# Kernel optimization log

Measured on AMD Instinct MI355X. Metric: run time of the kernel, lower is better.

## Reference

```python
import jax, jax.numpy as jnp
import numpy as np


def setup_inputs() -> dict:
    key = jax.random.key(0)
    ks = jax.random.split(key, 5)
    B, N, F, S = 8, 128, 32, 8
    F_ = 32          # output channels
    H = 32           # kernel_network hidden width
    node_features = jax.random.normal(ks[0], (B, N, F), dtype=jnp.float32)
    fltr = jax.random.uniform(ks[1], (B, N, N), dtype=jnp.float32)
    edge_features = jax.random.normal(ks[2], (B, N, N, S), dtype=jnp.float32)
    W0 = jax.random.normal(ks[3], (S, H), dtype=jnp.float32) * (1.0 / np.sqrt(S))
    b0 = jnp.zeros((H,), dtype=jnp.float32)
    W_out = jax.random.normal(ks[4], (H, F_ * F), dtype=jnp.float32) * (1.0 / np.sqrt(H))
    b_out = jnp.zeros((F_ * F,), dtype=jnp.float32)
    bias = jnp.zeros((F_,), dtype=jnp.float32)
    return {"node_features": node_features, "fltr": fltr, "edge_features": edge_features,
            "W0": W0, "b0": b0, "W_out": W_out, "b_out": b_out, "bias": bias}


def reference(node_features, fltr, edge_features, W0, b0, W_out, b_out, bias):
    B, N, F = node_features.shape
    F_ = bias.shape[0]
    # row-normalize the filter (adjacency)
    fltr_n = fltr / jnp.maximum(jnp.sum(fltr, axis=-1, keepdims=True), 1e-11)
    # kernel-generating network over edge features: (B,N,N,S) -> (B,N,N,F_*F)
    h = jax.nn.relu(edge_features @ W0 + b0)
    kernel = (h @ W_out + b_out).reshape(B, N, N, F_, F)
    # scale by normalized filter and aggregate neighbors:
    # out[a,b,c] = sum_{i,f} fltr_n[a,b,i] * kernel[a,b,i,c,f] * nf[a,i,f]
    out = jnp.einsum('abi,abicf,aif->abc', fltr_n, kernel, node_features)
    out = out + bias  # (B,N,F_)
    return out
```

## Files before the change

kernel.cpp:

```cpp
#include <hip/hip_runtime.h>

#define Bn 8
#define Nn 128
#define Fdim 32
#define Sdim 8
#define Hdim 32
#define Fout 32

typedef float  f32x4  __attribute__((ext_vector_type(4)));
typedef short  bf16x8 __attribute__((ext_vector_type(8)));

#define PITCH 136

__device__ __forceinline__ unsigned short f2bf(float x) {
    union { float f; unsigned u; } v; v.f = x;
    return (unsigned short)((v.u + 0x7FFFu + ((v.u >> 16) & 1u)) >> 16);
}
__device__ __forceinline__ unsigned pack2(float lo, float hi) {
    return (unsigned)f2bf(lo) | ((unsigned)f2bf(hi) << 16);
}

__global__ __launch_bounds__(256, 4) void ecc_kernel(
    const float* __restrict__ nf,
    const float* __restrict__ fltr,
    const float* __restrict__ ef,
    const float* __restrict__ W0,
    const float* __restrict__ b0,
    const float* __restrict__ Wout,
    const float* __restrict__ bout,
    const float* __restrict__ bias,
    float* __restrict__ out)
{
    __shared__ __align__(16) unsigned short hT[Hdim * PITCH];
    __shared__ __align__(16) unsigned short nT[Fdim * PITCH];
    __shared__ __align__(16) float Ts[Hdim * 36];
    __shared__ __align__(16) float qp[Nn];
    __shared__ float inv_s;

    const int t    = threadIdx.x;
    const int blk  = blockIdx.x;
    const int a    = blk >> 7;
    const int hcol = t & 31;

    const float* __restrict__ nfa  = nf   + (size_t)a   * (Nn * Fdim);
    const float* __restrict__ frow = fltr + (size_t)blk * Nn;
    const float* __restrict__ erow = ef   + (size_t)blk * (Nn * Sdim);

    float w0r[Sdim];
    #pragma unroll
    for (int s = 0; s < Sdim; ++s) w0r[s] = W0[s * Hdim + hcol];
    const float b0r = b0[hcol];

    if (t < 64) {
        float s = frow[t] + frow[t + 64];
        #pragma unroll
        for (int off = 32; off > 0; off >>= 1) s += __shfl_down(s, off);
        if (t == 0) inv_s = 1.0f / fmaxf(s, 1e-11f);
    }

    {
        const int f = t & 31, iseg = t >> 5;
        unsigned* dst = (unsigned*)&nT[f * PITCH + iseg * 16];
        #pragma unroll 4
        for (int k = 0; k < 16; k += 2) {
            const int i = iseg * 16 + k;
            const float x0 = nfa[i * Fdim + f];
            const float x1 = nfa[(i + 1) * Fdim + f];
            dst[k >> 1] = pack2(x0, x1);
        }
    }

    {
        const int il = t >> 5;
        unsigned* dst = (unsigned*)&hT[hcol * PITCH + il * 16];
        #pragma unroll 2
        for (int k = 0; k < 16; k += 2) {
            const int i0 = il * 16 + k;
            const float4 e0a = *(const float4*)(erow + i0 * Sdim);
            const float4 e0b = *(const float4*)(erow + i0 * Sdim + 4);
            const float4 e1a = *(const float4*)(erow + i0 * Sdim + 8);
            const float4 e1b = *(const float4*)(erow + i0 * Sdim + 12);
            float a0 = b0r, a1 = b0r;
            a0 += e0a.x * w0r[0] + e0a.y * w0r[1] + e0a.z * w0r[2] + e0a.w * w0r[3];
            a0 += e0b.x * w0r[4] + e0b.y * w0r[5] + e0b.z * w0r[6] + e0b.w * w0r[7];
            a1 += e1a.x * w0r[0] + e1a.y * w0r[1] + e1a.z * w0r[2] + e1a.w * w0r[3];
            a1 += e1b.x * w0r[4] + e1b.y * w0r[5] + e1b.z * w0r[6] + e1b.w * w0r[7];
            const float h0 = fmaxf(a0, 0.0f) * frow[i0];
            const float h1 = fmaxf(a1, 0.0f) * frow[i0 + 1];
            dst[k >> 1] = pack2(h0, h1);
        }
    }

    if (t >= 128) {
        const int f = t & 31, qr = (t >> 5) & 3;
        float q = 0.f;
        #pragma unroll 4
        for (int k = 0; k < 32; ++k) {
            const int i = qr * 32 + k;
            q += frow[i] * nfa[i * Fdim + f];
        }
        qp[qr * 32 + f] = q;
    }
    __syncthreads();

    {
        const int w  = t >> 6, l = t & 63;
        const int lr = l & 15, lg = l >> 4;
        const int mt = w >> 1, nt = w & 1;
        f32x4 acc = {0.f, 0.f, 0.f, 0.f};
        #pragma unroll
        for (int kt = 0; kt < 4; ++kt) {
            const bf16x8 av = *(const bf16x8*)&hT[(mt * 16 + lr) * PITCH + kt * 32 + lg * 8];
            const bf16x8 bv = *(const bf16x8*)&nT[(nt * 16 + lr) * PITCH + kt * 32 + lg * 8];
            acc = __builtin_amdgcn_mfma_f32_16x16x32_bf16(av, bv, acc, 0, 0, 0);
        }
        #pragma unroll
        for (int r = 0; r < 4; ++r)
            Ts[(mt * 16 + lg * 4 + r) * 36 + nt * 16 + lr] = acc[r];
    }
    __syncthreads();

    {
        const int c = t >> 3, f4 = t & 7;
        const float* wbase = Wout + (size_t)c * Fdim + f4 * 4;
        float partial = 0.f;
        #pragma unroll 8
        for (int h = 0; h < Hdim; ++h) {
            const float4 wv = *(const float4*)(wbase + (size_t)h * (Fout * Fdim));
            const float4 tv = *(const float4*)&Ts[h * 36 + f4 * 4];
            partial += tv.x * wv.x + tv.y * wv.y + tv.z * wv.z + tv.w * wv.w;
        }
        {
            const float4 q0 = *(const float4*)&qp[f4 * 4];
            const float4 q1 = *(const float4*)&qp[32 + f4 * 4];
            const float4 q2 = *(const float4*)&qp[64 + f4 * 4];
            const float4 q3 = *(const float4*)&qp[96 + f4 * 4];
            const float4 bv = *(const float4*)(bout + (size_t)c * Fdim + f4 * 4);
            partial += (q0.x + q1.x + q2.x + q3.x) * bv.x;
            partial += (q0.y + q1.y + q2.y + q3.y) * bv.y;
            partial += (q0.z + q1.z + q2.z + q3.z) * bv.z;
            partial += (q0.w + q1.w + q2.w + q3.w) * bv.w;
        }
        partial += __shfl_down(partial, 4, 8);
        partial += __shfl_down(partial, 2, 8);
        partial += __shfl_down(partial, 1, 8);
        if (f4 == 0)
            out[(size_t)blk * Fout + c] = partial * inv_s + bias[c];
    }
}

extern "C" void kernel_launch(void* const* d_in, const int* in_sizes, int n_in,
                              void* d_out, int out_size, void* d_ws, size_t ws_size,
                              hipStream_t stream) {
    const float* nf   = (const float*)d_in[0];
    const float* fltr = (const float*)d_in[1];
    const float* ef   = (const float*)d_in[2];
    const float* W0   = (const float*)d_in[3];
    const float* b0   = (const float*)d_in[4];
    const float* Wout = (const float*)d_in[5];
    const float* bout = (const float*)d_in[6];
    const float* bias = (const float*)d_in[7];
    float* out = (float*)d_out;

    ecc_kernel<<<dim3(Bn * Nn), dim3(256), 0, stream>>>(
        nf, fltr, ef, W0, b0, Wout, bout, bias, out);
}
```

Baseline: 80.89 us.

## Double block size to 512 threads and split MFMA K across waves

Each block now runs 512 threads, so every thread handles half as many rows in the staging phases. The node-feature staging is fused with the filter-weighted q reduction, which removes the separate q loop. The MFMA K dimension is split across two wave groups that combine their results with shared-memory atomicAdd into a zeroed Ts buffer. The final projection is re-split over h with a 16-lane shuffle reduction. This raises per-block parallelism and memory-level parallelism, but adds atomics, a zeroing pass, and possible occupancy limits from the larger blocks.

```diff
diff --git a/kernel.cpp b/kernel.cpp
--- a/kernel.cpp
+++ b/kernel.cpp
@@ -11,6 +11,7 @@
 typedef short  bf16x8 __attribute__((ext_vector_type(8)));
 
 #define PITCH 136
+#define TSP   36
 
 __device__ __forceinline__ unsigned short f2bf(float x) {
     union { float f; unsigned u; } v; v.f = x;
@@ -20,7 +21,7 @@
     return (unsigned)f2bf(lo) | ((unsigned)f2bf(hi) << 16);
 }
 
-__global__ __launch_bounds__(256, 4) void ecc_kernel(
+__global__ __launch_bounds__(512, 8) void ecc_kernel(
     const float* __restrict__ nf,
     const float* __restrict__ fltr,
     const float* __restrict__ ef,
@@ -33,14 +34,15 @@
 {
     __shared__ __align__(16) unsigned short hT[Hdim * PITCH];
     __shared__ __align__(16) unsigned short nT[Fdim * PITCH];
-    __shared__ __align__(16) float Ts[Hdim * 36];
-    __shared__ __align__(16) float qp[Nn];
+    __shared__ __align__(16) float Ts[Hdim * TSP];
+    __shared__ __align__(16) float qp[16 * Fdim];
     __shared__ float inv_s;
 
     const int t    = threadIdx.x;
     const int blk  = blockIdx.x;
     const int a    = blk >> 7;
     const int hcol = t & 31;
+    const int seg  = t >> 5;
 
     const float* __restrict__ nfa  = nf   + (size_t)a   * (Nn * Fdim);
     const float* __restrict__ frow = fltr + (size_t)blk * Nn;
@@ -58,24 +60,27 @@
         if (t == 0) inv_s = 1.0f / fmaxf(s, 1e-11f);
     }
 
+    if (t < (Hdim * TSP) / 4) ((f32x4*)Ts)[t] = (f32x4){0.f, 0.f, 0.f, 0.f};
+
     {
-        const int f = t & 31, iseg = t >> 5;
-        unsigned* dst = (unsigned*)&nT[f * PITCH + iseg * 16];
-        #pragma unroll 4
-        for (int k = 0; k < 16; k += 2) {
-            const int i = iseg * 16 + k;
-            const float x0 = nfa[i * Fdim + f];
-            const float x1 = nfa[(i + 1) * Fdim + f];
-            dst[k >> 1] = pack2(x0, x1);
+        float x[8], q = 0.f;
+        #pragma unroll
+        for (int k = 0; k < 8; ++k) {
+            const int i = seg * 8 + k;
+            x[k] = nfa[i * Fdim + hcol];
+            q += frow[i] * x[k];
         }
+        unsigned* dst = (unsigned*)&nT[hcol * PITCH + seg * 8];
+        #pragma unroll
+        for (int k = 0; k < 8; k += 2) dst[k >> 1] = pack2(x[k], x[k + 1]);
+        qp[seg * Fdim + hcol] = q;
     }
 
     {
-        const int il = t >> 5;
-        unsigned* dst = (unsigned*)&hT[hcol * PITCH + il * 16];
-        #pragma unroll 2
-        for (int k = 0; k < 16; k += 2) {
-            const int i0 = il * 16 + k;
+        unsigned* dst = (unsigned*)&hT[hcol * PITCH + seg * 8];
+        #pragma unroll 4
+        for (int k = 0; k < 8; k += 2) {
+            const int i0 = seg * 8 + k;
             const float4 e0a = *(const float4*)(erow + i0 * Sdim);
             const float4 e0b = *(const float4*)(erow + i0 * Sdim + 4);
             const float4 e1a = *(const float4*)(erow + i0 * Sdim + 8);
@@ -90,61 +95,55 @@
             dst[k >> 1] = pack2(h0, h1);
         }
     }
-
-    if (t >= 128) {
-        const int f = t & 31, qr = (t >> 5) & 3;
-        float q = 0.f;
-        #pragma unroll 4
-        for (int k = 0; k < 32; ++k) {
-            const int i = qr * 32 + k;
-            q += frow[i] * nfa[i * Fdim + f];
-        }
-        qp[qr * 32 + f] = q;
-    }
     __syncthreads();
 
     {
         const int w  = t >> 6, l = t & 63;
         const int lr = l & 15, lg = l >> 4;
-        const int mt = w >> 1, nt = w & 1;
+        const int tile = w & 3, kh = w >> 2;
+        const int mt = tile >> 1, nt = tile & 1;
         f32x4 acc = {0.f, 0.f, 0.f, 0.f};
         #pragma unroll
-        for (int kt = 0; kt < 4; ++kt) {
+        for (int kk = 0; kk < 2; ++kk) {
+            const int kt = kh * 2 + kk;
             const bf16x8 av = *(const bf16x8*)&hT[(mt * 16 + lr) * PITCH + kt * 32 + lg * 8];
             const bf16x8 bv = *(const bf16x8*)&nT[(nt * 16 + lr) * PITCH + kt * 32 + lg * 8];
             acc = __builtin_amdgcn_mfma_f32_16x16x32_bf16(av, bv, acc, 0, 0, 0);
         }
         #pragma unroll
         for (int r = 0; r < 4; ++r)
-            Ts[(mt * 16 + lg * 4 + r) * 36 + nt * 16 + lr] = acc[r];
+            atomicAdd(&Ts[(mt * 16 + lg * 4 + r) * TSP + nt * 16 + lr], acc[r]);
     }
     __syncthreads();
 
     {
-        const int c = t >> 3, f4 = t & 7;
-        const float* wbase = Wout + (size_t)c * Fdim + f4 * 4;
+        const int c = t >> 4, hp = t & 15;
         float partial = 0.f;
-        #pragma unroll 8
-        for (int h = 0; h < Hdim; ++h) {
-            const float4 wv = *(const float4*)(wbase + (size_t)h * (Fout * Fdim));
-            const float4 tv = *(const float4*)&Ts[h * 36 + f4 * 4];
-            partial += tv.x * wv.x + tv.y * wv.y + tv.z * wv.z + tv.w * wv.w;
+        #pragma unroll
+        for (int hh = 0; hh < 2; ++hh) {
+            const int h = hp + hh * 16;
+            const float* wbase = Wout + (size_t)h * (Fout * Fdim) + c * Fdim;
+            #pragma unroll 4
+            for (int f4 = 0; f4 < 8; ++f4) {
+                const float4 wv = *(const float4*)(wbase + f4 * 4);
+                const float4 tv = *(const float4*)&Ts[h * TSP + f4 * 4];
+                partial += tv.x * wv.x + tv.y * wv.y + tv.z * wv.z + tv.w * wv.w;
+            }
         }
         {
-            const float4 q0 = *(const float4*)&qp[f4 * 4];
-            const float4 q1 = *(const float4*)&qp[32 + f4 * 4];
-            const float4 q2 = *(const float4*)&qp[64 + f4 * 4];
-            const float4 q3 = *(const float4*)&qp[96 + f4 * 4];
-            const float4 bv = *(const float4*)(bout + (size_t)c * Fdim + f4 * 4);
-            partial += (q0.x + q1.x + q2.x + q3.x) * bv.x;
-            partial += (q0.y + q1.y + q2.y + q3.y) * bv.y;
-            partial += (q0.z + q1.z + q2.z + q3.z) * bv.z;
-            partial += (q0.w + q1.w + q2.w + q3.w) * bv.w;
+            const float* bbase = bout + (size_t)c * Fdim;
+            #pragma unroll 4
+            for (int f4 = 0; f4 < 8; ++f4) {
+                const float4 bv = *(const float4*)(bbase + f4 * 4);
+                const float4 qv = *(const float4*)&qp[hp * Fdim + f4 * 4];
+                partial += qv.x * bv.x + qv.y * bv.y + qv.z * bv.z + qv.w * bv.w;
+            }
         }
-        partial += __shfl_down(partial, 4, 8);
-        partial += __shfl_down(partial, 2, 8);
-        partial += __shfl_down(partial, 1, 8);
-        if (f4 == 0)
+        partial += __shfl_down(partial, 8, 16);
+        partial += __shfl_down(partial, 4, 16);
+        partial += __shfl_down(partial, 2, 16);
+        partial += __shfl_down(partial, 1, 16);
+        if (hp == 0)
             out[(size_t)blk * Fout + c] = partial * inv_s + bias[c];
     }
 }
@@ -162,6 +161,6 @@
     const float* bias = (const float*)d_in[7];
     float* out = (float*)d_out;
 
-    ecc_kernel<<<dim3(Bn * Nn), dim3(256), 0, stream>>>(
+    ecc_kernel<<<dim3(Bn * Nn), dim3(512), 0, stream>>>(
         nf, fltr, ef, W0, b0, Wout, bout, bias, out);
 }
```

After: 99.90 us. 23.5% more time.

## Split K across waves with per-wave MFMA tiles and LDS atomic reduction

Applied to the files above, without the earlier changes.

Each of the four waves now owns a 32-row slice of the neighbor dimension. It builds its own slice of hT and nT, with the q-vector folded into the nT load loop, runs a full 2x2 set of MFMAs over that slice, and reduces partial results into a shared accumulator with LDS atomicAdd. This replaces the sync between staging and MFMA with a wave-local lgkmcnt wait, and it raises the launch-bounds occupancy hint from 4 to 6. The cost is an extra zero-init barrier, many LDS float atomics, and a reduction order that is no longer deterministic.

```diff
diff --git a/kernel.cpp b/kernel.cpp
--- a/kernel.cpp
+++ b/kernel.cpp
@@ -7,10 +7,10 @@
 #define Hdim 32
 #define Fout 32
 
+#define QP 40
+
 typedef float  f32x4  __attribute__((ext_vector_type(4)));
 typedef short  bf16x8 __attribute__((ext_vector_type(8)));
-
-#define PITCH 136
 
 __device__ __forceinline__ unsigned short f2bf(float x) {
     union { float f; unsigned u; } v; v.f = x;
@@ -20,7 +20,7 @@
     return (unsigned)f2bf(lo) | ((unsigned)f2bf(hi) << 16);
 }
 
-__global__ __launch_bounds__(256, 4) void ecc_kernel(
+__global__ __launch_bounds__(256, 6) void ecc_kernel(
     const float* __restrict__ nf,
     const float* __restrict__ fltr,
     const float* __restrict__ ef,
@@ -31,16 +31,19 @@
     const float* __restrict__ bias,
     float* __restrict__ out)
 {
-    __shared__ __align__(16) unsigned short hT[Hdim * PITCH];
-    __shared__ __align__(16) unsigned short nT[Fdim * PITCH];
-    __shared__ __align__(16) float Ts[Hdim * 36];
-    __shared__ __align__(16) float qp[Nn];
-    __shared__ float inv_s;
+    __shared__ __align__(16) unsigned short hT[4 * Hdim * QP];
+    __shared__ __align__(16) unsigned short nT[4 * Fdim * QP];
+    __shared__ __align__(16) float Tacc[1056];
+    __shared__ float qsum[4];
 
-    const int t    = threadIdx.x;
-    const int blk  = blockIdx.x;
-    const int a    = blk >> 7;
-    const int hcol = t & 31;
+    const int t     = threadIdx.x;
+    const int blk   = blockIdx.x;
+    const int a     = blk >> 7;
+    const int w     = t >> 6;
+    const int l     = t & 63;
+    const int lane5 = l & 31;
+    const int ihalf = l >> 5;
+    const int i0    = w * 32;
 
     const float* __restrict__ nfa  = nf   + (size_t)a   * (Nn * Fdim);
     const float* __restrict__ frow = fltr + (size_t)blk * Nn;
@@ -48,104 +51,110 @@
 
     float w0r[Sdim];
     #pragma unroll
-    for (int s = 0; s < Sdim; ++s) w0r[s] = W0[s * Hdim + hcol];
-    const float b0r = b0[hcol];
+    for (int s = 0; s < Sdim; ++s) w0r[s] = W0[s * Hdim + lane5];
+    const float b0r = b0[lane5];
 
-    if (t < 64) {
-        float s = frow[t] + frow[t + 64];
+    {
+        f32x4 z = {0.f, 0.f, 0.f, 0.f};
+        ((f32x4*)Tacc)[t < 264 ? t : 0] = z;
+        if (t < 8) ((f32x4*)Tacc)[256 + t] = z;
+    }
+    __syncthreads();
+
+
+    {
+        float s = frow[i0 + lane5];
         #pragma unroll
-        for (int off = 32; off > 0; off >>= 1) s += __shfl_down(s, off);
-        if (t == 0) inv_s = 1.0f / fmaxf(s, 1e-11f);
+        for (int off = 16; off > 0; off >>= 1) s += __shfl_down(s, off, 32);
+        if (l == 0) qsum[w] = s;
     }
 
     {
-        const int f = t & 31, iseg = t >> 5;
-        unsigned* dst = (unsigned*)&nT[f * PITCH + iseg * 16];
-        #pragma unroll 4
-        for (int k = 0; k < 16; k += 2) {
-            const int i = iseg * 16 + k;
-            const float x0 = nfa[i * Fdim + f];
-            const float x1 = nfa[(i + 1) * Fdim + f];
-            dst[k >> 1] = pack2(x0, x1);
+        float x[16], qpart = 0.f;
+        #pragma unroll
+        for (int k = 0; k < 16; ++k) {
+            const int i = i0 + ihalf * 16 + k;
+            x[k] = nfa[i * Fdim + lane5];
+            qpart += frow[i] * x[k];
         }
+        unsigned* nd = (unsigned*)&nT[(size_t)(w * Fdim + lane5) * QP];
+        #pragma unroll
+        for (int k = 0; k < 16; k += 2) nd[ihalf * 8 + (k >> 1)] = pack2(x[k], x[k + 1]);
+        qpart += __shfl_xor(qpart, 32);
+        if (ihalf == 0) atomicAdd(&Tacc[1024 + lane5], qpart);
     }
 
     {
-        const int il = t >> 5;
-        unsigned* dst = (unsigned*)&hT[hcol * PITCH + il * 16];
-        #pragma unroll 2
+        unsigned* hd = (unsigned*)&hT[(size_t)(w * Hdim + lane5) * QP];
+        #pragma unroll
         for (int k = 0; k < 16; k += 2) {
-            const int i0 = il * 16 + k;
-            const float4 e0a = *(const float4*)(erow + i0 * Sdim);
-            const float4 e0b = *(const float4*)(erow + i0 * Sdim + 4);
-            const float4 e1a = *(const float4*)(erow + i0 * Sdim + 8);
-            const float4 e1b = *(const float4*)(erow + i0 * Sdim + 12);
+            const int i = i0 + ihalf * 16 + k;
+            const float4 e0a = *(const float4*)(erow + i * Sdim);
+            const float4 e0b = *(const float4*)(erow + i * Sdim + 4);
+            const float4 e1a = *(const float4*)(erow + i * Sdim + 8);
+            const float4 e1b = *(const float4*)(erow + i * Sdim + 12);
             float a0 = b0r, a1 = b0r;
             a0 += e0a.x * w0r[0] + e0a.y * w0r[1] + e0a.z * w0r[2] + e0a.w * w0r[3];
             a0 += e0b.x * w0r[4] + e0b.y * w0r[5] + e0b.z * w0r[6] + e0b.w * w0r[7];
             a1 += e1a.x * w0r[0] + e1a.y * w0r[1] + e1a.z * w0r[2] + e1a.w * w0r[3];
             a1 += e1b.x * w0r[4] + e1b.y * w0r[5] + e1b.z * w0r[6] + e1b.w * w0r[7];
-            const float h0 = fmaxf(a0, 0.0f) * frow[i0];
-            const float h1 = fmaxf(a1, 0.0f) * frow[i0 + 1];
-            dst[k >> 1] = pack2(h0, h1);
+            const float h0 = fmaxf(a0, 0.0f) * frow[i];
+            const float h1 = fmaxf(a1, 0.0f) * frow[i + 1];
+            hd[ihalf * 8 + (k >> 1)] = pack2(h0, h1);
         }
     }
 
-    if (t >= 128) {
-        const int f = t & 31, qr = (t >> 5) & 3;
-        float q = 0.f;
-        #pragma unroll 4
-        for (int k = 0; k < 32; ++k) {
-            const int i = qr * 32 + k;
-            q += frow[i] * nfa[i * Fdim + f];
+    asm volatile("s_waitcnt lgkmcnt(0)" ::: "memory");
+    __builtin_amdgcn_sched_barrier(0);
+
+    {
+        const int lr = l & 15, lg = l >> 4;
+        f32x4 acc[2][2];
+        #pragma unroll
+        for (int mt = 0; mt < 2; ++mt)
+            #pragma unroll
+            for (int nt = 0; nt < 2; ++nt) acc[mt][nt] = (f32x4){0.f, 0.f, 0.f, 0.f};
+        #pragma unroll
+        for (int mt = 0; mt < 2; ++mt) {
+            const bf16x8 av = *(const bf16x8*)&hT[(size_t)(w * Hdim + mt * 16 + lr) * QP + lg * 8];
+            #pragma unroll
+            for (int nt = 0; nt < 2; ++nt) {
+                const bf16x8 bv = *(const bf16x8*)&nT[(size_t)(w * Fdim + nt * 16 + lr) * QP + lg * 8];
+                acc[mt][nt] = __builtin_amdgcn_mfma_f32_16x16x32_bf16(av, bv, acc[mt][nt], 0, 0, 0);
+            }
         }
-        qp[qr * 32 + f] = q;
+        #pragma unroll
+        for (int mt = 0; mt < 2; ++mt)
+            #pragma unroll
+            for (int nt = 0; nt < 2; ++nt)
+                #pragma unroll
+                for (int r = 0; r < 4; ++r)
+                    atomicAdd(&Tacc[(mt * 16 + lg * 4 + r) * Fdim + nt * 16 + lr],
+                              acc[mt][nt][r]);
     }
     __syncthreads();
 
     {
-        const int w  = t >> 6, l = t & 63;
-        const int lr = l & 15, lg = l >> 4;
-        const int mt = w >> 1, nt = w & 1;
-        f32x4 acc = {0.f, 0.f, 0.f, 0.f};
-        #pragma unroll
-        for (int kt = 0; kt < 4; ++kt) {
-            const bf16x8 av = *(const bf16x8*)&hT[(mt * 16 + lr) * PITCH + kt * 32 + lg * 8];
-            const bf16x8 bv = *(const bf16x8*)&nT[(nt * 16 + lr) * PITCH + kt * 32 + lg * 8];
-            acc = __builtin_amdgcn_mfma_f32_16x16x32_bf16(av, bv, acc, 0, 0, 0);
-        }
-        #pragma unroll
-        for (int r = 0; r < 4; ++r)
-            Ts[(mt * 16 + lg * 4 + r) * 36 + nt * 16 + lr] = acc[r];
-    }
-    __syncthreads();
-
-    {
+        const float inv = 1.0f / fmaxf(qsum[0] + qsum[1] + qsum[2] + qsum[3], 1e-11f);
         const int c = t >> 3, f4 = t & 7;
         const float* wbase = Wout + (size_t)c * Fdim + f4 * 4;
         float partial = 0.f;
-        #pragma unroll 8
+        #pragma unroll
         for (int h = 0; h < Hdim; ++h) {
             const float4 wv = *(const float4*)(wbase + (size_t)h * (Fout * Fdim));
-            const float4 tv = *(const float4*)&Ts[h * 36 + f4 * 4];
+            const float4 tv = *(const float4*)&Tacc[h * Fdim + f4 * 4];
             partial += tv.x * wv.x + tv.y * wv.y + tv.z * wv.z + tv.w * wv.w;
         }
         {
-            const float4 q0 = *(const float4*)&qp[f4 * 4];
-            const float4 q1 = *(const float4*)&qp[32 + f4 * 4];
-            const float4 q2 = *(const float4*)&qp[64 + f4 * 4];
-            const float4 q3 = *(const float4*)&qp[96 + f4 * 4];
             const float4 bv = *(const float4*)(bout + (size_t)c * Fdim + f4 * 4);
-            partial += (q0.x + q1.x + q2.x + q3.x) * bv.x;
-            partial += (q0.y + q1.y + q2.y + q3.y) * bv.y;
-            partial += (q0.z + q1.z + q2.z + q3.z) * bv.z;
-            partial += (q0.w + q1.w + q2.w + q3.w) * bv.w;
+            const float4 qv = *(const float4*)&Tacc[1024 + f4 * 4];
+            partial += qv.x * bv.x + qv.y * bv.y + qv.z * bv.z + qv.w * bv.w;
         }
         partial += __shfl_down(partial, 4, 8);
         partial += __shfl_down(partial, 2, 8);
         partial += __shfl_down(partial, 1, 8);
         if (f4 == 0)
-            out[(size_t)blk * Fout + c] = partial * inv_s + bias[c];
+            out[(size_t)blk * Fout + c] = partial * inv + bias[c];
     }
 }
 
```

Result: slower. 97.89 us (+21.0%).
